# Kernel optimization log

Hardware: AMD Instinct MI355X
Metric: run time of the kernel (lower is better)

The kernel has to match this reference:

```python
import jax, jax.numpy as jnp
import numpy as np

WS = (4, 4, 4)          # window size (D, H, W)
DIM = 96
HEADS = 8
HEAD_DIM = DIM // HEADS
SCALE = HEAD_DIM ** (-0.5)
N = WS[0] * WS[1] * WS[2]  # 64 tokens per window


def _relative_position_index(ws):
    coords = np.stack(np.meshgrid(np.arange(ws[0]), np.arange(ws[1]), np.arange(ws[2]), indexing='ij'))
    cf = coords.reshape(3, -1)                       # [3, N]
    rel = cf[:, :, None] - cf[:, None, :]            # [3, N, N]
    rel = rel.transpose(1, 2, 0).astype(np.int64)    # [N, N, 3]
    rel[:, :, 0] += ws[0] - 1
    rel[:, :, 1] += ws[1] - 1
    rel[:, :, 2] += ws[2] - 1
    rel[:, :, 0] *= (2 * ws[1] - 1) * (2 * ws[2] - 1)
    rel[:, :, 1] *= 2 * ws[2] - 1
    return jnp.asarray(rel.sum(-1))                  # [N, N]

REL_IDX = _relative_position_index(WS)


def setup_inputs() -> dict:
    key = jax.random.key(0)
    ks = jax.random.split(key, 6)
    B = 4096   # total windows (64 images x 64 windows)
    nW = 64
    table_size = (2 * WS[0] - 1) * (2 * WS[1] - 1) * (2 * WS[2] - 1)  # 343
    return {
        'x': jax.random.normal(ks[0], (B, N, DIM), jnp.float32),
        'mask': jax.random.normal(ks[1], (nW, N, N), jnp.float32),
        'qkv_w': jax.random.normal(ks[2], (3 * DIM, DIM), jnp.float32) * 0.02,
        'proj_w': jax.random.normal(ks[3], (DIM, DIM), jnp.float32) * 0.02,
        'proj_b': jnp.zeros((DIM,), jnp.float32),
        'bias_table': jax.random.normal(ks[4], (table_size, HEADS), jnp.float32) * 0.02,
    }


def reference(x, mask, qkv_w, proj_w, proj_b, bias_table):
    B, n, C = x.shape
    # QKV projection (torch Linear: y = x @ W.T), split into heads
    qkv = (x @ qkv_w.T).reshape(B, n, 3, HEADS, HEAD_DIM)
    qkv = jnp.transpose(qkv, (2, 0, 3, 1, 4))        # [3, B, H, N, hd]
    q, k, v = qkv[0], qkv[1], qkv[2]
    attn = jnp.einsum('bhnd,bhmd->bhnm', q, k) * SCALE
    # gathered relative position bias: [N, N, H] -> [H, N, N]
    bias = bias_table[REL_IDX[:n, :n].reshape(-1)].reshape(n, n, HEADS)
    attn = attn + jnp.transpose(bias, (2, 0, 1))[None]
    # shifted-window mask add
    nW = mask.shape[0]
    attn = attn.reshape(B // nW, nW, HEADS, n, n) + mask[None, :, None]
    attn = attn.reshape(B, HEADS, n, n)
    attn = jax.nn.softmax(attn, axis=-1)
    out = jnp.einsum('bhnm,bhmd->bnhd', attn, v).reshape(B, n, C)
    return out @ proj_w.T + proj_b
```

## Files before the change

kernel.cpp:

```cpp
#include <hip/hip_runtime.h>
#include <stdint.h>


typedef float  f32x4  __attribute__((ext_vector_type(4)));
typedef __fp16 f16x2  __attribute__((ext_vector_type(2)));
typedef __fp16 f16x4  __attribute__((ext_vector_type(4)));
typedef __fp16 f16x8  __attribute__((ext_vector_type(8)));

#define WS_WQKVP_OFF  (8388608)
#define WS_WPROJT_OFF (8388608 + 73728)
#define LOG2E 1.4426950408889634f

__device__ __forceinline__ f16x4 pk4(f32x4 v) {
  union { f16x2 p[2]; f16x4 v; } u;
  u.p[0] = __builtin_amdgcn_cvt_pkrtz(v[0], v[1]);
  u.p[1] = __builtin_amdgcn_cvt_pkrtz(v[2], v[3]);
  return u.v;
}

__global__ void prep_weights(const float* __restrict__ qkv_w,
                             const float* __restrict__ proj_w,
                             __fp16* __restrict__ wsh) {
  int tid = blockIdx.x * 256 + threadIdx.x;
  if (tid < 36864) {
    int h = tid / 4608, rem = tid - h * 4608;
    int s = rem / 1536, rem2 = rem - s * 1536;
    int r = rem2 / 96, cc = rem2 - r * 96;
    float v = 0.f;
    if (r < 12) {
      v = qkv_w[(s * 96 + h * 12 + r) * 96 + cc];
      if (s == 0) v *= (0.28867513459481288f * LOG2E);
    }
    wsh[WS_WQKVP_OFF / 2 + tid] = (__fp16)v;
  } else {
    int t = tid - 36864;
    int h = t / 1536, rem = t - h * 1536;
    int o = rem >> 4, c = rem & 15;
    float v = (c < 12) ? proj_w[o * 96 + h * 12 + c] : 0.f;
    wsh[WS_WPROJT_OFF / 2 + t] = (__fp16)v;
  }
}

__global__ void prep_biasm(const float* __restrict__ mask,
                           const float* __restrict__ bias_table,
                           float* __restrict__ biasm) {
  int tid = blockIdx.x * 256 + threadIdx.x;
  int m = tid & 63;
  int r = (tid >> 6) & 63;
  int h = (tid >> 12) & 7;
  int w = tid >> 15;
  int dr = r >> 4, hr = (r >> 2) & 3, wr = r & 3;
  int dm = m >> 4, hm = (m >> 2) & 3, wm = m & 3;
  int idx = (dr - dm + 3) * 49 + (hr - hm + 3) * 7 + (wr - wm + 3);
  biasm[tid] = (bias_table[idx * 8 + h] + mask[(w * 64 + r) * 64 + m]) * LOG2E;
}

__global__ __launch_bounds__(512, 4) void attn_main(
    const float* __restrict__ x, const float* __restrict__ proj_b,
    const __fp16* __restrict__ wsh, const float* __restrict__ biasm,
    float* __restrict__ out) {
  __shared__ __fp16 v_lds[8][16][68];
  __shared__ __fp16 o_lds[8][64][24];

  const int tid  = threadIdx.x;
  const int wv   = tid >> 6;
  const int lane = tid & 63;
  const int lo4 = lane & 15, hi4 = lane >> 4;
  const int blk = blockIdx.x;
  const int wmask = blk & 63;

  const __fp16* wq  = wsh + WS_WQKVP_OFF / 2 + wv * (3 * 16 * 96);
  const __fp16* wpT = wsh + WS_WPROJT_OFF / 2;

  f32x4 a1[3][4];
#pragma unroll
  for (int s = 0; s < 3; ++s)
#pragma unroll
    for (int tt = 0; tt < 4; ++tt) a1[s][tt] = (f32x4){0.f, 0.f, 0.f, 0.f};
  {
    const float* xw = x + (size_t)blk * 6144;
#pragma unroll
    for (int ks = 0; ks < 3; ++ks) {
      f16x8 bx[4];
#pragma unroll
      for (int tt = 0; tt < 4; ++tt) {
        const float* p = &xw[(tt * 16 + lo4) * 96 + ks * 32 + hi4 * 8];
        float4 v0 = *(const float4*)p;
        float4 v1 = *(const float4*)(p + 4);
        union { f16x2 h2[4]; f16x8 v; } u;
        u.h2[0] = __builtin_amdgcn_cvt_pkrtz(v0.x, v0.y);
        u.h2[1] = __builtin_amdgcn_cvt_pkrtz(v0.z, v0.w);
        u.h2[2] = __builtin_amdgcn_cvt_pkrtz(v1.x, v1.y);
        u.h2[3] = __builtin_amdgcn_cvt_pkrtz(v1.z, v1.w);
        bx[tt] = u.v;
      }
#pragma unroll
      for (int s = 0; s < 3; ++s) {
        f16x8 aw = *(const f16x8*)&wq[(s * 16 + lo4) * 96 + ks * 32 + hi4 * 8];
#pragma unroll
        for (int tt = 0; tt < 4; ++tt)
          a1[s][tt] = __builtin_amdgcn_mfma_f32_16x16x32_f16(aw, bx[tt], a1[s][tt], 0, 0, 0);
      }
    }
  }

  f16x4 Qf[4], Kf[4];
#pragma unroll
  for (int tt = 0; tt < 4; ++tt) {
    Qf[tt] = pk4(a1[0][tt]);
    Kf[tt] = pk4(a1[1][tt]);
#pragma unroll
    for (int j = 0; j < 4; ++j)
      v_lds[wv][hi4 * 4 + j][tt * 16 + lo4] = (__fp16)a1[2][tt][j];
  }

  f32x4 c[4][4];
  {
    const float* bm = biasm + (size_t)(wmask * 8 + wv) * 4096;
#pragma unroll
    for (int qt = 0; qt < 4; ++qt)
#pragma unroll
      for (int mt = 0; mt < 4; ++mt)
        c[mt][qt] = *(const f32x4*)&bm[(qt * 16 + lo4) * 64 + mt * 16 + hi4 * 4];
  }

  __builtin_amdgcn_s_setprio(1);
#pragma unroll
  for (int mt = 0; mt < 4; ++mt)
#pragma unroll
    for (int qt = 0; qt < 4; ++qt)
      c[mt][qt] = __builtin_amdgcn_mfma_f32_16x16x16f16(Kf[mt], Qf[qt], c[mt][qt], 0, 0, 0);
  __builtin_amdgcn_s_setprio(0);

#pragma unroll
  for (int qt = 0; qt < 4; ++qt) {
    float mx = -1e30f;
#pragma unroll
    for (int mt = 0; mt < 4; ++mt)
#pragma unroll
      for (int j = 0; j < 4; ++j) mx = fmaxf(mx, c[mt][qt][j]);
    mx = fmaxf(mx, __shfl_xor(mx, 16));
    mx = fmaxf(mx, __shfl_xor(mx, 32));
    float sum = 0.f;
#pragma unroll
    for (int mt = 0; mt < 4; ++mt)
#pragma unroll
      for (int j = 0; j < 4; ++j) {
        float e = exp2f(c[mt][qt][j] - mx);
        c[mt][qt][j] = e;
        sum += e;
      }
    sum += __shfl_xor(sum, 16);
    sum += __shfl_xor(sum, 32);
    float rs = 1.0f / sum;
#pragma unroll
    for (int mt = 0; mt < 4; ++mt)
#pragma unroll
      for (int j = 0; j < 4; ++j) c[mt][qt][j] *= rs;
  }

  f16x4 pa[4][4];
#pragma unroll
  for (int qt = 0; qt < 4; ++qt)
#pragma unroll
    for (int mt = 0; mt < 4; ++mt) pa[qt][mt] = pk4(c[mt][qt]);
  f16x4 vb[4];
#pragma unroll
  for (int mt = 0; mt < 4; ++mt)
    vb[mt] = *(const f16x4*)&v_lds[wv][lo4][mt * 16 + hi4 * 4];

  f32x4 o4[4];
#pragma unroll
  for (int qt = 0; qt < 4; ++qt) o4[qt] = (f32x4){0.f, 0.f, 0.f, 0.f};
  __builtin_amdgcn_s_setprio(1);
#pragma unroll
  for (int mt = 0; mt < 4; ++mt)
#pragma unroll
    for (int qt = 0; qt < 4; ++qt)
      o4[qt] = __builtin_amdgcn_mfma_f32_16x16x16f16(pa[qt][mt], vb[mt], o4[qt], 0, 0, 0);
  __builtin_amdgcn_s_setprio(0);

  const int mt3 = wv >> 1;
  const int nb3 = (wv & 1) * 3;
  const int arow3 = mt3 * 16 + lo4;
  const int hh3 = hi4 >> 1;
  const int off8 = (hi4 & 1) * 8;
  f16x8 wf[12];
#pragma unroll
  for (int ks = 0; ks < 4; ++ks)
#pragma unroll
    for (int nt = 0; nt < 3; ++nt)
      wf[ks * 3 + nt] = *(const f16x8*)
          &wpT[((size_t)(ks * 2 + hh3) * 96 + (nb3 + nt) * 16 + lo4) * 16 + off8];

#pragma unroll
  for (int qt = 0; qt < 4; ++qt)
#pragma unroll
    for (int j = 0; j < 4; ++j)
      o_lds[wv][qt * 16 + hi4 * 4 + j][lo4] = (__fp16)o4[qt][j];

  __syncthreads();

  {
    f32x4 acc[3];
#pragma unroll
    for (int nt = 0; nt < 3; ++nt) acc[nt] = (f32x4){0.f, 0.f, 0.f, 0.f};
#pragma unroll
    for (int ks = 0; ks < 4; ++ks) {
      f16x8 af = *(const f16x8*)&o_lds[ks * 2 + hh3][arow3][off8];
#pragma unroll
      for (int nt = 0; nt < 3; ++nt)
        acc[nt] = __builtin_amdgcn_mfma_f32_16x16x32_f16(af, wf[ks * 3 + nt], acc[nt], 0, 0, 0);
    }
    float* od = out + (size_t)blk * 6144;
#pragma unroll
    for (int nt = 0; nt < 3; ++nt) {
      const int ntg = nb3 + nt;
      float pb = proj_b[ntg * 16 + lo4];
#pragma unroll
      for (int j = 0; j < 4; ++j)
        od[(mt3 * 16 + hi4 * 4 + j) * 96 + ntg * 16 + lo4] = acc[nt][j] + pb;
    }
  }
}

extern "C" void kernel_launch(void* const* d_in, const int* in_sizes, int n_in,
                              void* d_out, int out_size, void* d_ws, size_t ws_size,
                              hipStream_t stream) {
  const float* x          = (const float*)d_in[0];
  const float* mask       = (const float*)d_in[1];
  const float* qkv_w      = (const float*)d_in[2];
  const float* proj_w     = (const float*)d_in[3];
  const float* proj_b     = (const float*)d_in[4];
  const float* bias_table = (const float*)d_in[5];

  float* biasm = (float*)d_ws;
  __fp16* wsh = (__fp16*)d_ws;

  prep_weights<<<192, 256, 0, stream>>>(qkv_w, proj_w, wsh);
  prep_biasm<<<8192, 256, 0, stream>>>(mask, bias_table, biasm);
  attn_main<<<4096, 512, 0, stream>>>(x, proj_b, wsh, biasm, (float*)d_out);
}
```

Measured before the change: 193.1 us.

## Stage x tile in LDS once per window and process two windows per block

Before, each of the 8 waves read and converted the whole fp32 x window from global memory on its own. Now the block loads x once with coalesced float4 reads, converts it to fp16, and stores it in a shared xs buffer that the QKV MFMAs read from. Each block also loops over two windows, so the grid is halved. In exchange there is an extra __syncthreads per window and more LDS per block, which may lower occupancy, and the two-window loop serialises work inside each block.

New measurement: 264.0 us. 1.37x slower.

```diff
diff --git a/kernel.cpp b/kernel.cpp
--- a/kernel.cpp
+++ b/kernel.cpp
@@ -16,6 +16,11 @@
   u.p[0] = __builtin_amdgcn_cvt_pkrtz(v[0], v[1]);
   u.p[1] = __builtin_amdgcn_cvt_pkrtz(v[2], v[3]);
   return u.v;
+}
+__device__ __forceinline__ uint32_t pku(float a, float b) {
+  union { f16x2 p; uint32_t u; } u;
+  u.p = __builtin_amdgcn_cvt_pkrtz(a, b);
+  return u.u;
 }
 
 __global__ void prep_weights(const float* __restrict__ qkv_w,
@@ -59,6 +64,7 @@
     const float* __restrict__ x, const float* __restrict__ proj_b,
     const __fp16* __restrict__ wsh, const float* __restrict__ biasm,
     float* __restrict__ out) {
+  __shared__ __fp16 xs[64][104];
   __shared__ __fp16 v_lds[8][16][68];
   __shared__ __fp16 o_lds[8][64][24];
 
@@ -67,159 +73,165 @@
   const int lane = tid & 63;
   const int lo4 = lane & 15, hi4 = lane >> 4;
   const int blk = blockIdx.x;
-  const int wmask = blk & 63;
 
   const __fp16* wq  = wsh + WS_WQKVP_OFF / 2 + wv * (3 * 16 * 96);
   const __fp16* wpT = wsh + WS_WPROJT_OFF / 2;
-
-  f32x4 a1[3][4];
-#pragma unroll
-  for (int s = 0; s < 3; ++s)
-#pragma unroll
-    for (int tt = 0; tt < 4; ++tt) a1[s][tt] = (f32x4){0.f, 0.f, 0.f, 0.f};
-  {
-    const float* xw = x + (size_t)blk * 6144;
-#pragma unroll
-    for (int ks = 0; ks < 3; ++ks) {
-      f16x8 bx[4];
-#pragma unroll
-      for (int tt = 0; tt < 4; ++tt) {
-        const float* p = &xw[(tt * 16 + lo4) * 96 + ks * 32 + hi4 * 8];
-        float4 v0 = *(const float4*)p;
-        float4 v1 = *(const float4*)(p + 4);
-        union { f16x2 h2[4]; f16x8 v; } u;
-        u.h2[0] = __builtin_amdgcn_cvt_pkrtz(v0.x, v0.y);
-        u.h2[1] = __builtin_amdgcn_cvt_pkrtz(v0.z, v0.w);
-        u.h2[2] = __builtin_amdgcn_cvt_pkrtz(v1.x, v1.y);
-        u.h2[3] = __builtin_amdgcn_cvt_pkrtz(v1.z, v1.w);
-        bx[tt] = u.v;
-      }
-#pragma unroll
-      for (int s = 0; s < 3; ++s) {
-        f16x8 aw = *(const f16x8*)&wq[(s * 16 + lo4) * 96 + ks * 32 + hi4 * 8];
-#pragma unroll
-        for (int tt = 0; tt < 4; ++tt)
-          a1[s][tt] = __builtin_amdgcn_mfma_f32_16x16x32_f16(aw, bx[tt], a1[s][tt], 0, 0, 0);
-      }
-    }
-  }
-
-  f16x4 Qf[4], Kf[4];
-#pragma unroll
-  for (int tt = 0; tt < 4; ++tt) {
-    Qf[tt] = pk4(a1[0][tt]);
-    Kf[tt] = pk4(a1[1][tt]);
-#pragma unroll
-    for (int j = 0; j < 4; ++j)
-      v_lds[wv][hi4 * 4 + j][tt * 16 + lo4] = (__fp16)a1[2][tt][j];
-  }
-
-  f32x4 c[4][4];
-  {
-    const float* bm = biasm + (size_t)(wmask * 8 + wv) * 4096;
-#pragma unroll
-    for (int qt = 0; qt < 4; ++qt)
-#pragma unroll
-      for (int mt = 0; mt < 4; ++mt)
-        c[mt][qt] = *(const f32x4*)&bm[(qt * 16 + lo4) * 64 + mt * 16 + hi4 * 4];
-  }
-
-  __builtin_amdgcn_s_setprio(1);
-#pragma unroll
-  for (int mt = 0; mt < 4; ++mt)
-#pragma unroll
-    for (int qt = 0; qt < 4; ++qt)
-      c[mt][qt] = __builtin_amdgcn_mfma_f32_16x16x16f16(Kf[mt], Qf[qt], c[mt][qt], 0, 0, 0);
-  __builtin_amdgcn_s_setprio(0);
-
-#pragma unroll
-  for (int qt = 0; qt < 4; ++qt) {
-    float mx = -1e30f;
-#pragma unroll
-    for (int mt = 0; mt < 4; ++mt)
-#pragma unroll
-      for (int j = 0; j < 4; ++j) mx = fmaxf(mx, c[mt][qt][j]);
-    mx = fmaxf(mx, __shfl_xor(mx, 16));
-    mx = fmaxf(mx, __shfl_xor(mx, 32));
-    float sum = 0.f;
-#pragma unroll
-    for (int mt = 0; mt < 4; ++mt)
-#pragma unroll
-      for (int j = 0; j < 4; ++j) {
-        float e = exp2f(c[mt][qt][j] - mx);
-        c[mt][qt][j] = e;
-        sum += e;
-      }
-    sum += __shfl_xor(sum, 16);
-    sum += __shfl_xor(sum, 32);
-    float rs = 1.0f / sum;
-#pragma unroll
-    for (int mt = 0; mt < 4; ++mt)
-#pragma unroll
-      for (int j = 0; j < 4; ++j) c[mt][qt][j] *= rs;
-  }
-
-  f16x4 pa[4][4];
-#pragma unroll
-  for (int qt = 0; qt < 4; ++qt)
-#pragma unroll
-    for (int mt = 0; mt < 4; ++mt) pa[qt][mt] = pk4(c[mt][qt]);
-  f16x4 vb[4];
-#pragma unroll
-  for (int mt = 0; mt < 4; ++mt)
-    vb[mt] = *(const f16x4*)&v_lds[wv][lo4][mt * 16 + hi4 * 4];
-
-  f32x4 o4[4];
-#pragma unroll
-  for (int qt = 0; qt < 4; ++qt) o4[qt] = (f32x4){0.f, 0.f, 0.f, 0.f};
-  __builtin_amdgcn_s_setprio(1);
-#pragma unroll
-  for (int mt = 0; mt < 4; ++mt)
-#pragma unroll
-    for (int qt = 0; qt < 4; ++qt)
-      o4[qt] = __builtin_amdgcn_mfma_f32_16x16x16f16(pa[qt][mt], vb[mt], o4[qt], 0, 0, 0);
-  __builtin_amdgcn_s_setprio(0);
 
   const int mt3 = wv >> 1;
   const int nb3 = (wv & 1) * 3;
   const int arow3 = mt3 * 16 + lo4;
   const int hh3 = hi4 >> 1;
   const int off8 = (hi4 & 1) * 8;
-  f16x8 wf[12];
-#pragma unroll
-  for (int ks = 0; ks < 4; ++ks)
-#pragma unroll
-    for (int nt = 0; nt < 3; ++nt)
-      wf[ks * 3 + nt] = *(const f16x8*)
-          &wpT[((size_t)(ks * 2 + hh3) * 96 + (nb3 + nt) * 16 + lo4) * 16 + off8];
-
-#pragma unroll
-  for (int qt = 0; qt < 4; ++qt)
-#pragma unroll
-    for (int j = 0; j < 4; ++j)
-      o_lds[wv][qt * 16 + hi4 * 4 + j][lo4] = (__fp16)o4[qt][j];
-
-  __syncthreads();
-
-  {
-    f32x4 acc[3];
-#pragma unroll
-    for (int nt = 0; nt < 3; ++nt) acc[nt] = (f32x4){0.f, 0.f, 0.f, 0.f};
-#pragma unroll
-    for (int ks = 0; ks < 4; ++ks) {
-      f16x8 af = *(const f16x8*)&o_lds[ks * 2 + hh3][arow3][off8];
+
+  for (int w2 = 0; w2 < 2; ++w2) {
+    const int win = blk * 2 + w2;
+    const int wmask = win & 63;
+
+    {
+      const float4* xw = (const float4*)(x + (size_t)win * 6144);
+      for (int i = tid; i < 1536; i += 512) {
+        float4 v = xw[i];
+        int t = i / 24, c4 = (i % 24) * 4;
+        uint2 p;
+        p.x = pku(v.x, v.y);
+        p.y = pku(v.z, v.w);
+        *(uint2*)&xs[t][c4] = p;
+      }
+    }
+    __syncthreads();
+
+    f32x4 a1[3][4];
+#pragma unroll
+    for (int s = 0; s < 3; ++s)
+#pragma unroll
+      for (int tt = 0; tt < 4; ++tt) a1[s][tt] = (f32x4){0.f, 0.f, 0.f, 0.f};
+#pragma unroll
+    for (int ks = 0; ks < 3; ++ks) {
+      f16x8 bx[4];
+#pragma unroll
+      for (int tt = 0; tt < 4; ++tt)
+        bx[tt] = *(const f16x8*)&xs[tt * 16 + lo4][ks * 32 + hi4 * 8];
+#pragma unroll
+      for (int s = 0; s < 3; ++s) {
+        f16x8 aw = *(const f16x8*)&wq[(s * 16 + lo4) * 96 + ks * 32 + hi4 * 8];
+#pragma unroll
+        for (int tt = 0; tt < 4; ++tt)
+          a1[s][tt] = __builtin_amdgcn_mfma_f32_16x16x32_f16(aw, bx[tt], a1[s][tt], 0, 0, 0);
+      }
+    }
+
+    f16x4 Qf[4], Kf[4];
+#pragma unroll
+    for (int tt = 0; tt < 4; ++tt) {
+      Qf[tt] = pk4(a1[0][tt]);
+      Kf[tt] = pk4(a1[1][tt]);
+#pragma unroll
+      for (int j = 0; j < 4; ++j)
+        v_lds[wv][hi4 * 4 + j][tt * 16 + lo4] = (__fp16)a1[2][tt][j];
+    }
+
+    f32x4 c[4][4];
+    {
+      const float* bm = biasm + (size_t)(wmask * 8 + wv) * 4096;
+#pragma unroll
+      for (int qt = 0; qt < 4; ++qt)
+#pragma unroll
+        for (int mt = 0; mt < 4; ++mt)
+          c[mt][qt] = *(const f32x4*)&bm[(qt * 16 + lo4) * 64 + mt * 16 + hi4 * 4];
+    }
+
+    __builtin_amdgcn_s_setprio(1);
+#pragma unroll
+    for (int mt = 0; mt < 4; ++mt)
+#pragma unroll
+      for (int qt = 0; qt < 4; ++qt)
+        c[mt][qt] = __builtin_amdgcn_mfma_f32_16x16x16f16(Kf[mt], Qf[qt], c[mt][qt], 0, 0, 0);
+    __builtin_amdgcn_s_setprio(0);
+
+#pragma unroll
+    for (int qt = 0; qt < 4; ++qt) {
+      float mx = -1e30f;
+#pragma unroll
+      for (int mt = 0; mt < 4; ++mt)
+#pragma unroll
+        for (int j = 0; j < 4; ++j) mx = fmaxf(mx, c[mt][qt][j]);
+      mx = fmaxf(mx, __shfl_xor(mx, 16));
+      mx = fmaxf(mx, __shfl_xor(mx, 32));
+      float sum = 0.f;
+#pragma unroll
+      for (int mt = 0; mt < 4; ++mt)
+#pragma unroll
+        for (int j = 0; j < 4; ++j) {
+          float e = exp2f(c[mt][qt][j] - mx);
+          c[mt][qt][j] = e;
+          sum += e;
+        }
+      sum += __shfl_xor(sum, 16);
+      sum += __shfl_xor(sum, 32);
+      float rs = 1.0f / sum;
+#pragma unroll
+      for (int mt = 0; mt < 4; ++mt)
+#pragma unroll
+        for (int j = 0; j < 4; ++j) c[mt][qt][j] *= rs;
+    }
+
+    f16x4 pa[4][4];
+#pragma unroll
+    for (int qt = 0; qt < 4; ++qt)
+#pragma unroll
+      for (int mt = 0; mt < 4; ++mt) pa[qt][mt] = pk4(c[mt][qt]);
+    f16x4 vb[4];
+#pragma unroll
+    for (int mt = 0; mt < 4; ++mt)
+      vb[mt] = *(const f16x4*)&v_lds[wv][lo4][mt * 16 + hi4 * 4];
+
+    f32x4 o4[4];
+#pragma unroll
+    for (int qt = 0; qt < 4; ++qt) o4[qt] = (f32x4){0.f, 0.f, 0.f, 0.f};
+    __builtin_amdgcn_s_setprio(1);
+#pragma unroll
+    for (int mt = 0; mt < 4; ++mt)
+#pragma unroll
+      for (int qt = 0; qt < 4; ++qt)
+        o4[qt] = __builtin_amdgcn_mfma_f32_16x16x16f16(pa[qt][mt], vb[mt], o4[qt], 0, 0, 0);
+    __builtin_amdgcn_s_setprio(0);
+
+    f16x8 wf[12];
+#pragma unroll
+    for (int ks = 0; ks < 4; ++ks)
 #pragma unroll
       for (int nt = 0; nt < 3; ++nt)
-        acc[nt] = __builtin_amdgcn_mfma_f32_16x16x32_f16(af, wf[ks * 3 + nt], acc[nt], 0, 0, 0);
-    }
-    float* od = out + (size_t)blk * 6144;
-#pragma unroll
-    for (int nt = 0; nt < 3; ++nt) {
-      const int ntg = nb3 + nt;
-      float pb = proj_b[ntg * 16 + lo4];
+        wf[ks * 3 + nt] = *(const f16x8*)
+            &wpT[((size_t)(ks * 2 + hh3) * 96 + (nb3 + nt) * 16 + lo4) * 16 + off8];
+
+#pragma unroll
+    for (int qt = 0; qt < 4; ++qt)
 #pragma unroll
       for (int j = 0; j < 4; ++j)
-        od[(mt3 * 16 + hi4 * 4 + j) * 96 + ntg * 16 + lo4] = acc[nt][j] + pb;
+        o_lds[wv][qt * 16 + hi4 * 4 + j][lo4] = (__fp16)o4[qt][j];
+
+    __syncthreads();
+
+    {
+      f32x4 acc[3];
+#pragma unroll
+      for (int nt = 0; nt < 3; ++nt) acc[nt] = (f32x4){0.f, 0.f, 0.f, 0.f};
+#pragma unroll
+      for (int ks = 0; ks < 4; ++ks) {
+        f16x8 af = *(const f16x8*)&o_lds[ks * 2 + hh3][arow3][off8];
+#pragma unroll
+        for (int nt = 0; nt < 3; ++nt)
+          acc[nt] = __builtin_amdgcn_mfma_f32_16x16x32_f16(af, wf[ks * 3 + nt], acc[nt], 0, 0, 0);
+      }
+      float* od = out + (size_t)win * 6144;
+#pragma unroll
+      for (int nt = 0; nt < 3; ++nt) {
+        const int ntg = nb3 + nt;
+        float pb = proj_b[ntg * 16 + lo4];
+#pragma unroll
+        for (int j = 0; j < 4; ++j)
+          od[(mt3 * 16 + hi4 * 4 + j) * 96 + ntg * 16 + lo4] = acc[nt][j] + pb;
+      }
     }
   }
 }
@@ -239,5 +251,5 @@
 
   prep_weights<<<192, 256, 0, stream>>>(qkv_w, proj_w, wsh);
   prep_biasm<<<8192, 256, 0, stream>>>(mask, bias_table, biasm);
-  attn_main<<<4096, 512, 0, stream>>>(x, proj_b, wsh, biasm, (float*)d_out);
-}
+  attn_main<<<2048, 512, 0, stream>>>(x, proj_b, wsh, biasm, (float*)d_out);
+}
```
